# Kernel tuning notes

Measured on AMD Instinct MI355X. Metric: run time of the kernel, lower is better.

Reference implementation:

```python
import jax, jax.numpy as jnp
import numpy as np

B, T, I, H = 2048, 512, 9, 56


def _lstm_layer(x, w_ih, w_hh, b_ih, b_hh):
    """Single LSTM layer, batch_first x: [B, T, in] -> [B, T, H].
    PyTorch gate order: i, f, g, o."""
    # Precompute input projections for all timesteps in one GEMM: [B, T, 4H]
    xp = jnp.einsum('bti,gi->btg', x, w_ih) + b_ih + b_hh
    xp_t = jnp.transpose(xp, (1, 0, 2))  # [T, B, 4H]
    h0 = jnp.zeros((x.shape[0], w_hh.shape[1]), dtype=x.dtype)
    c0 = jnp.zeros_like(h0)

    def step(carry, xt):
        h, c = carry
        gates = xt + h @ w_hh.T  # [B, 4H]
        i, f, g, o = jnp.split(gates, 4, axis=-1)
        i = jax.nn.sigmoid(i)
        f = jax.nn.sigmoid(f)
        g = jnp.tanh(g)
        o = jax.nn.sigmoid(o)
        c = f * c + i * g
        h = o * jnp.tanh(c)
        return (h, c), h

    _, hs = jax.lax.scan(step, (h0, c0), xp_t)  # hs: [T, B, H]
    return jnp.transpose(hs, (1, 0, 2))  # [B, T, H]


def setup_inputs() -> dict:
    key = jax.random.key(0)
    ks = jax.random.split(key, 13)
    s_in = 1.0 / np.sqrt(H)
    inp = {
        'x': jax.random.normal(ks[0], (B, T, I), dtype=jnp.float32),
        'w_ih0': jax.random.uniform(ks[1], (4 * H, I), jnp.float32, -s_in, s_in),
        'w_hh0': jax.random.uniform(ks[2], (4 * H, H), jnp.float32, -s_in, s_in),
        'b_ih0': jax.random.uniform(ks[3], (4 * H,), jnp.float32, -s_in, s_in),
        'b_hh0': jax.random.uniform(ks[4], (4 * H,), jnp.float32, -s_in, s_in),
        'w_ih1': jax.random.uniform(ks[5], (4 * H, H), jnp.float32, -s_in, s_in),
        'w_hh1': jax.random.uniform(ks[6], (4 * H, H), jnp.float32, -s_in, s_in),
        'b_ih1': jax.random.uniform(ks[7], (4 * H,), jnp.float32, -s_in, s_in),
        'b_hh1': jax.random.uniform(ks[8], (4 * H,), jnp.float32, -s_in, s_in),
        'fc1_w': jax.random.uniform(ks[9], (H // 2, H), jnp.float32, -s_in, s_in),
        'fc1_b': jax.random.uniform(ks[10], (H // 2,), jnp.float32, -s_in, s_in),
        'fc2_w': jax.random.uniform(ks[11], (1, H // 2), jnp.float32, -0.2, 0.2),
        'fc2_b': jax.random.uniform(ks[12], (1,), jnp.float32, -0.2, 0.2),
    }
    return inp


def reference(x, w_ih0, w_hh0, b_ih0, b_hh0, w_ih1, w_hh1, b_ih1, b_hh1,
              fc1_w, fc1_b, fc2_w, fc2_b):
    h = _lstm_layer(x, w_ih0, w_hh0, b_ih0, b_hh0)   # [B, T, H]
    h = _lstm_layer(h, w_ih1, w_hh1, b_ih1, b_hh1)   # [B, T, H]
    last = h[:, -1]                                   # [B, H]
    y = jax.nn.relu(last @ fc1_w.T + fc1_b)           # [B, H//2]
    return y @ fc2_w.T + fc2_b                        # [B, 1]
```

## Files before the change

kernel.cpp:

```cpp
#include <hip/hip_runtime.h>
#include <stdint.h>

#define T_LEN 512
#define IN0   9
#define H     56
#define BG    8
#define NW    8
#define NTH   (NW * 64)
#define NBLK  256

typedef __attribute__((ext_vector_type(8))) short bfrag;
typedef __attribute__((ext_vector_type(4))) float ffrag;

#define MFMA(a,b,c) __builtin_amdgcn_mfma_f32_16x16x32_bf16((a),(b),(c),0,0,0)

__device__ __forceinline__ uint32_t bf16hi(float x) {
  uint32_t u = __float_as_uint(x);
  return (u + 0x7FFFu + ((u >> 16) & 1u)) & 0xFFFF0000u;
}
__device__ __forceinline__ void split_bf16(float x, short& hs, short& ls) {
  uint32_t hb = bf16hi(x);
  float lf = x - __uint_as_float(hb);
  hs = (short)(hb >> 16);
  ls = (short)(bf16hi(lf) >> 16);
}
__device__ __forceinline__ void split_bf16t(float x, short& hs, short& ls) {
  uint32_t hb = bf16hi(x);
  float lf = x - __uint_as_float(hb);
  hs = (short)(hb >> 16);
  ls = (short)(__float_as_uint(lf) >> 16);
}
__device__ __forceinline__ float dpp8(float v) {
  return __int_as_float(__builtin_amdgcn_update_dpp(0, __float_as_int(v), 0x128, 0xF, 0xF, true));
}
__device__ __forceinline__ float rcp_f(float v)  { return __builtin_amdgcn_rcpf(v); }
__device__ __forceinline__ float sigm_f(float v) { return rcp_f(1.0f + __expf(-v)); }
__device__ __forceinline__ float tanh_f(float v) { return 1.0f - 2.0f * rcp_f(1.0f + __expf(2.0f * v)); }

__global__ __launch_bounds__(NTH, 2)
void lstm_mfma12(const float* __restrict__ x,
                 const float* __restrict__ w_ih0, const float* __restrict__ w_hh0,
                 const float* __restrict__ b_ih0, const float* __restrict__ b_hh0,
                 const float* __restrict__ w_ih1, const float* __restrict__ w_hh1,
                 const float* __restrict__ b_ih1, const float* __restrict__ b_hh1,
                 const float* __restrict__ fc1_w, const float* __restrict__ fc1_b,
                 const float* __restrict__ fc2_w, const float* __restrict__ fc2_b,
                 float* __restrict__ out)
{
  __shared__ __align__(16) short hbufS[4 * 1024];
  __shared__ __align__(16) short xfS[T_LEN * 128];
  __shared__ __align__(16) float x8S[T_LEN * BG];
  __shared__ float sF[BG * H];
  __shared__ float sY[BG * 28];

  const int tid  = threadIdx.x;
  const int lane = tid & 63;
  const int w    = tid >> 6;
  const int c16  = lane & 15;
  const int quad = lane >> 4;

  const bool HASB = (w < 6);
  const int  sBi  = HASB ? (8 + w) : 0;

  for (int i = tid; i < 2048; i += NTH) ((int*)hbufS)[i] = 0;

  const int lay = (lane >> 3) & 1;
  const int b   = lane & 7;

  bfrag B0hA[2], B0lA[2], BuhA[2], BhhA[2];
  bfrag B0hB[2], B0lB[2], BuhB[2], BhhB[2];

#define LOADA(SUF, SIDX)                                                        \
  {                                                                             \
    const int np_ = 16 * (SIDX) + c16;                                          \
    const int jb_ = np_ >> 2, gb_ = np_ & 3;                                    \
    const int wrow_ = gb_ * H + jb_;                                            \
    _Pragma("unroll")                                                           \
    for (int s = 0; s < 2; ++s) {                                               \
      union { short sh[8]; bfrag v; } a0h, a0l, auh, ahh;                       \
      _Pragma("unroll")                                                         \
      for (int jj = 0; jj < 8; ++jj) {                                          \
        const int k = 32 * s + quad * 8 + jj;                                   \
        const float w0 = (k < H) ? w_hh0[wrow_ * H + k]                         \
                                 : w_ih0[wrow_ * IN0 + (k - 56)];               \
        const float wu = (k < H) ? w_ih1[wrow_ * H + k] : 0.0f;                 \
        const float wh = (k < H) ? w_hh1[wrow_ * H + k] : 0.0f;                 \
        split_bf16(w0, a0h.sh[jj], a0l.sh[jj]);                                 \
        short dum;                                                              \
        split_bf16(wu, auh.sh[jj], dum);                       \
        split_bf16(wh, ahh.sh[jj], dum);                                        \
      }                                                                         \
      B0h##SUF[s] = a0h.v; B0l##SUF[s] = a0l.v;                                 \
      Buh##SUF[s] = auh.v; Bhh##SUF[s] = ahh.v;                                 \
    }                                                                           \
  }

  LOADA(A, w)
  LOADA(B, sBi)
#undef LOADA

  const int j4A = 4 * w + quad;
  const int j4B = 4 * sBi + quad;
  const ffrag zerof = { 0.f, 0.f, 0.f, 0.f };

#define SETUPS(SUF, J4)                                                         \
  ffrag bias0f##SUF, bias1f##SUF;                                               \
  _Pragma("unroll")                                                             \
  for (int r = 0; r < 4; ++r) {                                                 \
    const float v0 = b_ih0[r * H + (J4)] + b_hh0[r * H + (J4)];                 \
    const float v1 = b_ih1[r * H + (J4)] + b_hh1[r * H + (J4)];                 \
    bias0f##SUF[r] = (c16 < 8) ? v0 : 0.0f;                                     \
    bias1f##SUF[r] = (c16 < 8) ? v1 : 0.0f;                                     \
  }                                                                             \
  float wx8a##SUF[4];                                                           \
  _Pragma("unroll")                                                             \
  for (int r = 0; r < 4; ++r)                                                   \
    wx8a##SUF[r] = lay ? w_ih0[(r * H + (J4)) * IN0 + 8] : 0.0f;                \
  const int kk##SUF = (J4) & 31;                                                \
  const int offE##SUF = ((J4) >> 5) * 512 + ((kk##SUF >> 3) * 16 + b) * 8       \
                        + (kk##SUF & 7);                                        \
  short* const hp0##SUF = hbufS + (lay ? 0 : 3 * 1024) + offE##SUF;             \
  short* const hp1##SUF = hbufS + (lay ? 1 * 1024 : 2 * 1024) + offE##SUF;

  SETUPS(A, j4A)
  SETUPS(B, j4B)
#undef SETUPS

  for (int item = tid; item < T_LEN * BG; item += NTH) {
    const int t  = item & (T_LEN - 1);
    const int bb = item >> 9;
    const float* xr = x + ((size_t)(blockIdx.x * BG + bb) * T_LEN + t) * IN0;
    union { short s[8]; bfrag v; } hi, lo;
    #pragma unroll
    for (int q = 0; q < 8; ++q) split_bf16t(xr[q], hi.s[q], lo.s[q]);
    *(bfrag*)((char*)xfS + (size_t)t * 256 + bb * 16)       = hi.v;
    *(bfrag*)((char*)xfS + (size_t)t * 256 + (bb + 8) * 16) = lo.v;
    x8S[t * 8 + bb] = xr[8];
  }

  const char* const hB = (const char*)hbufS;
  const char* const pU0_0 = hB + 2048 + lane * 16;
  const char* const pU0_1 = hB +        lane * 16;
  const char* const pH0_0 = hB + 4096 + lane * 16;
  const char* const pH1_0 = hB + 5120 + lane * 16;
  const char* const pH0_1 = hB + 6144 + lane * 16;
  const char* const pH1_1 = hB + 7168 + lane * 16;
  const char* pU1_0 = (quad == 3) ? ((const char*)xfS + 256 * 1 + c16 * 16)
                                  : (hB + 3072 + lane * 16);
  const char* pU1_1 = (quad == 3) ? ((const char*)xfS + 256 * 2 + c16 * 16)
                                  : (hB + 1024 + lane * 16);
  const char* px8_0 = (const char*)x8S + 32 * 1 + b * 4;
  const char* px8_1 = (const char*)x8S + 32 * 2 + b * 4;
  const int incU1 = (quad == 3) ? 512 : 0;

  float cstA = 0.f, cstB = 0.f;
  __syncthreads();

#define ACT0(A0, WX8, CST, HBP, X8V)                                            \
  {                                                                             \
    float s0[4];                                                                \
    _Pragma("unroll")                                                           \
    for (int r = 0; r < 4; ++r) s0[r] = A0[r] + dpp8(A0[r]);                    \
    if (lay) {                                                                  \
      const float gi = fmaf(WX8[0], X8V, s0[0]);                                \
      const float gf = fmaf(WX8[1], X8V, s0[1]);                                \
      const float gg = fmaf(WX8[2], X8V, s0[2]);                                \
      const float go = fmaf(WX8[3], X8V, s0[3]);                                \
      const float iv = sigm_f(gi), fv = sigm_f(gf);                             \
      const float gv = tanh_f(gg), ov = sigm_f(go);                             \
      CST = fmaf(fv, CST, iv * gv);                                             \
      const float hv = ov * tanh_f(CST);                                        \
      short hs, hl; split_bf16t(hv, hs, hl);                                    \
      (HBP)[0] = hs; (HBP)[64] = hl;                                            \
    }                                                                           \
  }

#define ACT1(A0A, A0B, AH, WX8, CST, HBP, X8V)                                  \
  {                                                                             \
    float sv[4];                                                                \
    _Pragma("unroll")                                                           \
    for (int r = 0; r < 4; ++r) {                                               \
      const float t0 = A0A[r] + A0B[r];                                         \
      const float uu = lay ? t0 : AH[r];                                        \
      const float vv = lay ? AH[r] : t0;                                        \
      sv[r] = uu + dpp8(vv);                                                    \
    }                                                                           \
    const float gi = fmaf(WX8[0], X8V, sv[0]);                                  \
    const float gf = fmaf(WX8[1], X8V, sv[1]);                                  \
    const float gg = fmaf(WX8[2], X8V, sv[2]);                                  \
    const float go = fmaf(WX8[3], X8V, sv[3]);                                  \
    const float iv = sigm_f(gi), fv = sigm_f(gf);                               \
    const float gv = tanh_f(gg), ov = sigm_f(go);                               \
    CST = fmaf(fv, CST, iv * gv);                                               \
    const float hv = ov * tanh_f(CST);                                          \
    short hs, hl; split_bf16t(hv, hs, hl);                                      \
    (HBP)[0] = hs; (HBP)[64] = hl;                                              \
  }

#define ACTL(AH, CST, J4)                                                       \
  {                                                                             \
    float s1[4];                                                                \
    _Pragma("unroll")                                                           \
    for (int r = 0; r < 4; ++r) s1[r] = AH[r] + dpp8(AH[r]);                    \
    if (lay == 0) {                                                             \
      const float iv = sigm_f(s1[0]), fv = sigm_f(s1[1]);                       \
      const float gv = tanh_f(s1[2]), ov = sigm_f(s1[3]);                       \
      CST = fmaf(fv, CST, iv * gv);                                             \
      sF[b * H + (J4)] = ov * tanh_f(CST);                                      \
    }                                                                           \
  }

  {
    const bfrag U0 = *(const bfrag*)(hB + lane * 16);
    const char* pU1p = (quad == 3) ? ((const char*)xfS + c16 * 16)
                                   : (hB + 1024 + lane * 16);
    const bfrag U1 = *(const bfrag*)pU1p;
    const float x8v = x8S[b];
    ffrag a0A = MFMA(B0hA[0], U0, bias0fA);
    a0A = MFMA(B0hA[1], U1, a0A);
    a0A = MFMA(B0lA[0], U0, a0A);
    a0A = MFMA(B0lA[1], U1, a0A);
    ACT0(a0A, wx8aA, cstA, hp1A, x8v)
    if (HASB) {
      ffrag a0B = MFMA(B0hB[0], U0, bias0fB);
      a0B = MFMA(B0hB[1], U1, a0B);
      a0B = MFMA(B0lB[0], U0, a0B);
      a0B = MFMA(B0lB[1], U1, a0B);
      ACT0(a0B, wx8aB, cstB, hp1B, x8v)
    }
    __syncthreads();
  }

#define REGION(RR, L0PART, LASTR)                                               \
  {                                                                             \
    const bfrag U0 = *(const bfrag*)pU0_##RR;                                   \
    const bfrag U1 = *(const bfrag*)pU1_##RR;                                   \
    const bfrag H0 = *(const bfrag*)pH0_##RR;                                   \
    const bfrag H1 = *(const bfrag*)pH1_##RR;                                   \
    ffrag a0aA, a0bA, a0aB, a0bB;                                               \
    float x8v = 0.0f;                                                           \
    if (L0PART) x8v = *(const float*)px8_##RR;                                  \
    __builtin_amdgcn_s_setprio(1);                                              \
    if (L0PART) {                                                               \
      a0aA = MFMA(B0hA[0], U0, bias0fA);                                        \
      a0bA = MFMA(B0lA[0], U0, zerof);                                          \
      a0aA = MFMA(B0hA[1], U1, a0aA);                                           \
      a0bA = MFMA(B0lA[1], U1, a0bA);                                           \
      if (HASB) {                                                               \
        a0aB = MFMA(B0hB[0], U0, bias0fB);                                      \
        a0bB = MFMA(B0lB[0], U0, zerof);                                        \
        a0aB = MFMA(B0hB[1], U1, a0aB);                                         \
        a0bB = MFMA(B0lB[1], U1, a0bB);                                         \
      }                                                                         \
    }                                                                           \
          \
    ffrag aHA = MFMA(BhhA[0], H0, bias1fA);                                     \
    aHA = MFMA(BhhA[1], H1, aHA);                                               \
    aHA = MFMA(BuhA[0], U0, aHA);                                               \
    aHA = MFMA(BuhA[1], U1, aHA);                                               \
    ffrag aHB;                                                                  \
    if (HASB) {                                                                 \
      aHB = MFMA(BhhB[0], H0, bias1fB);                                         \
      aHB = MFMA(BhhB[1], H1, aHB);                                             \
      aHB = MFMA(BuhB[0], U0, aHB);                                             \
      aHB = MFMA(BuhB[1], U1, aHB);                                             \
    }                                                                           \
    __builtin_amdgcn_s_setprio(0);                                              \
    if (!LASTR) {                                                               \
      ACT1(a0aA, a0bA, aHA, wx8aA, cstA, ((RR) == 0) ? hp0A : hp1A, x8v)        \
      if (HASB) {                                                               \
        ACT1(a0aB, a0bB, aHB, wx8aB, cstB, ((RR) == 0) ? hp0B : hp1B, x8v)      \
      }                                                                         \
    } else {                                                                    \
      ACTL(aHA, cstA, j4A)                                                      \
      if (HASB) { ACTL(aHB, cstB, j4B) }                                        \
    }                                                                           \
    __syncthreads();                                                            \
  }

  for (int it = 0; it < 255; ++it) {
    REGION(0, 1, 0)
    REGION(1, 1, 0)
    pU1_0 += incU1; pU1_1 += incU1;
    px8_0 += 64;    px8_1 += 64;
  }
  REGION(0, 1, 0)
  pU1_1 -= incU1;
  REGION(1, 0, 1)
#undef REGION
#undef ACT0
#undef ACT1
#undef ACTL

  if (tid < 28 * BG) {
    const int m  = tid >> 3;
    const int bb = tid & 7;
    float acc = fc1_b[m];
    const float4* w4 = (const float4*)(fc1_w + m * H);
    const float4* h4 = (const float4*)(sF + bb * H);
    #pragma unroll
    for (int qq = 0; qq < H / 4; ++qq) {
      const float4 wv4 = w4[qq], hv4 = h4[qq];
      acc = fmaf(wv4.x, hv4.x, acc);
      acc = fmaf(wv4.y, hv4.y, acc);
      acc = fmaf(wv4.z, hv4.z, acc);
      acc = fmaf(wv4.w, hv4.w, acc);
    }
    sY[bb * 28 + m] = fmaxf(acc, 0.0f);
  }
  __syncthreads();
  if (tid < BG) {
    float acc = fc2_b[0];
    #pragma unroll
    for (int m = 0; m < 28; ++m)
      acc = fmaf(fc2_w[m], sY[tid * 28 + m], acc);
    out[blockIdx.x * BG + tid] = acc;
  }
}

extern "C" void kernel_launch(void* const* d_in, const int* in_sizes, int n_in,
                              void* d_out, int out_size, void* d_ws, size_t ws_size,
                              hipStream_t stream)
{
  const float* x     = (const float*)d_in[0];
  const float* w_ih0 = (const float*)d_in[1];
  const float* w_hh0 = (const float*)d_in[2];
  const float* b_ih0 = (const float*)d_in[3];
  const float* b_hh0 = (const float*)d_in[4];
  const float* w_ih1 = (const float*)d_in[5];
  const float* w_hh1 = (const float*)d_in[6];
  const float* b_ih1 = (const float*)d_in[7];
  const float* b_hh1 = (const float*)d_in[8];
  const float* fc1_w = (const float*)d_in[9];
  const float* fc1_b = (const float*)d_in[10];
  const float* fc2_w = (const float*)d_in[11];
  const float* fc2_b = (const float*)d_in[12];
  float* out = (float*)d_out;

  lstm_mfma12<<<NBLK, NTH, 0, stream>>>(
      x, w_ih0, w_hh0, b_ih0, b_hh0, w_ih1, w_hh1, b_ih1, b_hh1,
      fc1_w, fc1_b, fc2_w, fc2_b, out);
}
```

Before: 476.1 us.

## Process 16 batch rows per block with two ping-ponged wave groups

New measurement: 1.448 ms. 3.04x slower.

```diff
diff --git a/kernel.cpp b/kernel.cpp
--- a/kernel.cpp
+++ b/kernel.cpp
@@ -4,10 +4,10 @@
 #define T_LEN 512
 #define IN0   9
 #define H     56
-#define BG    8
-#define NW    8
+#define BG    16
+#define NW    14
 #define NTH   (NW * 64)
-#define NBLK  256
+#define NBLK  (2048 / BG)
 
 typedef __attribute__((ext_vector_type(8))) short bfrag;
 typedef __attribute__((ext_vector_type(4))) float ffrag;
@@ -38,7 +38,7 @@
 __device__ __forceinline__ float tanh_f(float v) { return 1.0f - 2.0f * rcp_f(1.0f + __expf(2.0f * v)); }
 
 __global__ __launch_bounds__(NTH, 2)
-void lstm_mfma12(const float* __restrict__ x,
+void lstm_mfma16(const float* __restrict__ x,
                  const float* __restrict__ w_ih0, const float* __restrict__ w_hh0,
                  const float* __restrict__ b_ih0, const float* __restrict__ b_hh0,
                  const float* __restrict__ w_ih1, const float* __restrict__ w_hh1,
@@ -47,9 +47,9 @@
                  const float* __restrict__ fc2_w, const float* __restrict__ fc2_b,
                  float* __restrict__ out)
 {
-  __shared__ __align__(16) short hbufS[4 * 1024];
-  __shared__ __align__(16) short xfS[T_LEN * 128];
-  __shared__ __align__(16) float x8S[T_LEN * BG];
+  __shared__ __align__(16) short hbufS[2 * 4096];
+  __shared__ __align__(16) short xstgS[2 * 2 * 128];
+  __shared__ __align__(16) float x8S[BG * T_LEN];
   __shared__ float sF[BG * H];
   __shared__ float sY[BG * 28];
 
@@ -59,22 +59,23 @@
   const int c16  = lane & 15;
   const int quad = lane >> 4;
 
-  const bool HASB = (w < 6);
-  const int  sBi  = HASB ? (8 + w) : 0;
-
-  for (int i = tid; i < 2048; i += NTH) ((int*)hbufS)[i] = 0;
-
-  const int lay = (lane >> 3) & 1;
-  const int b   = lane & 7;
+  const int  grp = (w >= 7);
+  const int  wg  = grp ? (w - 7) : w;
+  const bool wgz = (wg == 0);
+  const int  lay = (lane >> 3) & 1;
+  const int  b   = lane & 7;
+  const int  bg16 = grp * 8 + b;
+  const int  sA = 2 * wg, sB = 2 * wg + 1;
+  const int  j4A = 4 * sA + quad, j4B = 4 * sB + quad;
+
+  for (int i = tid; i < 4096; i += NTH) ((int*)hbufS)[i] = 0;
 
   bfrag B0hA[2], B0lA[2], BuhA[2], BhhA[2];
   bfrag B0hB[2], B0lB[2], BuhB[2], BhhB[2];
-
-#define LOADA(SUF, SIDX)                                                        \
+#define LOADW(SUF, SIDX)                                                        \
   {                                                                             \
     const int np_ = 16 * (SIDX) + c16;                                          \
-    const int jb_ = np_ >> 2, gb_ = np_ & 3;                                    \
-    const int wrow_ = gb_ * H + jb_;                                            \
+    const int wrow_ = (np_ & 3) * H + (np_ >> 2);                               \
     _Pragma("unroll")                                                           \
     for (int s = 0; s < 2; ++s) {                                               \
       union { short sh[8]; bfrag v; } a0h, a0l, auh, ahh;                       \
@@ -94,15 +95,11 @@
       Buh##SUF[s] = auh.v; Bhh##SUF[s] = ahh.v;                                 \
     }                                                                           \
   }
-
-  LOADA(A, w)
-  LOADA(B, sBi)
-#undef LOADA
-
-  const int j4A = 4 * w + quad;
-  const int j4B = 4 * sBi + quad;
+  LOADW(A, sA)
+  LOADW(B, sB)
+#undef LOADW
+
   const ffrag zerof = { 0.f, 0.f, 0.f, 0.f };
-
 #define SETUPS(SUF, J4)                                                         \
   ffrag bias0f##SUF, bias1f##SUF;                                               \
   _Pragma("unroll")                                                             \
@@ -118,60 +115,86 @@
     wx8a##SUF[r] = lay ? w_ih0[(r * H + (J4)) * IN0 + 8] : 0.0f;                \
   const int kk##SUF = (J4) & 31;                                                \
   const int offE##SUF = ((J4) >> 5) * 512 + ((kk##SUF >> 3) * 16 + b) * 8       \
-                        + (kk##SUF & 7);                                        \
-  short* const hp0##SUF = hbufS + (lay ? 0 : 3 * 1024) + offE##SUF;             \
-  short* const hp1##SUF = hbufS + (lay ? 1 * 1024 : 2 * 1024) + offE##SUF;
-
+                        + (kk##SUF & 7);
   SETUPS(A, j4A)
   SETUPS(B, j4B)
 #undef SETUPS
 
-  for (int item = tid; item < T_LEN * BG; item += NTH) {
-    const int t  = item & (T_LEN - 1);
-    const int bb = item >> 9;
-    const float* xr = x + ((size_t)(blockIdx.x * BG + bb) * T_LEN + t) * IN0;
-    union { short s[8]; bfrag v; } hi, lo;
-    #pragma unroll
-    for (int q = 0; q < 8; ++q) split_bf16t(xr[q], hi.s[q], lo.s[q]);
-    *(bfrag*)((char*)xfS + (size_t)t * 256 + bb * 16)       = hi.v;
-    *(bfrag*)((char*)xfS + (size_t)t * 256 + (bb + 8) * 16) = lo.v;
-    x8S[t * 8 + bb] = xr[8];
-  }
-
-  const char* const hB = (const char*)hbufS;
-  const char* const pU0_0 = hB + 2048 + lane * 16;
-  const char* const pU0_1 = hB +        lane * 16;
-  const char* const pH0_0 = hB + 4096 + lane * 16;
-  const char* const pH1_0 = hB + 5120 + lane * 16;
-  const char* const pH0_1 = hB + 6144 + lane * 16;
-  const char* const pH1_1 = hB + 7168 + lane * 16;
-  const char* pU1_0 = (quad == 3) ? ((const char*)xfS + 256 * 1 + c16 * 16)
-                                  : (hB + 3072 + lane * 16);
-  const char* pU1_1 = (quad == 3) ? ((const char*)xfS + 256 * 2 + c16 * 16)
-                                  : (hB + 1024 + lane * 16);
-  const char* px8_0 = (const char*)x8S + 32 * 1 + b * 4;
-  const char* px8_1 = (const char*)x8S + 32 * 2 + b * 4;
-  const int incU1 = (quad == 3) ? 512 : 0;
-
+  const int gBs = grp * 4096;
+  short* const hwA0 = hbufS + gBs + (lay ? 0 * 1024 : 2048 + 1024) + offEA;
+  short* const hwA1 = hbufS + gBs + (lay ? 1 * 1024 : 2048 + 0)    + offEA;
+  short* const hwB0 = hbufS + gBs + (lay ? 0 * 1024 : 2048 + 1024) + offEB;
+  short* const hwB1 = hbufS + gBs + (lay ? 1 * 1024 : 2048 + 0)    + offEB;
+
+  const char* const hBb = (const char*)hbufS + grp * 8192;
+  const char* const xsb = (const char*)xstgS + grp * 512;
+  const char* const pU0_0 = hBb + 1 * 2048 + lane * 16;
+  const char* const pU0_1 = hBb + 0 * 2048 + lane * 16;
+  const char* const pU1_0 = (quad == 3) ? (xsb + 0 * 256 + c16 * 16) : (pU0_0 + 1024);
+  const char* const pU1_1 = (quad == 3) ? (xsb + 1 * 256 + c16 * 16) : (pU0_1 + 1024);
+  const char* const pH0_0 = hBb + 4096 + 0 * 2048 + lane * 16;
+  const char* const pH0_1 = hBb + 4096 + 1 * 2048 + lane * 16;
+
+  const int sb_ = (lane >> 2) & 7, se_ = lane & 3;
+  uint32_t* const xw_0 = (uint32_t*)((char*)xstgS + grp * 512 + 0 * 256 + sb_ * 16 + 4 * se_);
+  uint32_t* const xw_1 = (uint32_t*)((char*)xstgS + grp * 512 + 1 * 256 + sb_ * 16 + 4 * se_);
+  const float* xgp = x + ((size_t)(blockIdx.x * BG + grp * 8 + sb_) * T_LEN + 1) * IN0 + 2 * se_;
+
+  for (int item = tid; item < BG * T_LEN; item += NTH) {
+    const int bb = item >> 9, t = item & (T_LEN - 1);
+    x8S[item] = x[((size_t)(blockIdx.x * BG + bb) * T_LEN + t) * IN0 + 8];
+  }
+  if (wgz && lane < 32) {
+    const float* g0 = x + ((size_t)(blockIdx.x * BG + grp * 8 + sb_) * T_LEN) * IN0 + 2 * se_;
+    const float xa = g0[0], xb = g0[1];
+    short ah_, al_, bh_, bl_;
+    split_bf16t(xa, ah_, al_); split_bf16t(xb, bh_, bl_);
+    xw_0[0]  = (uint16_t)ah_ | ((uint32_t)(uint16_t)bh_ << 16);
+    xw_0[32] = (uint16_t)al_ | ((uint32_t)(uint16_t)bl_ << 16);
+  }
+
+  const float* const px8 = x8S + (size_t)bg16 * T_LEN;
   float cstA = 0.f, cstB = 0.f;
-  __syncthreads();
-
-#define ACT0(A0, WX8, CST, HBP, X8V)                                            \
-  {                                                                             \
-    float s0[4];                                                                \
-    _Pragma("unroll")                                                           \
-    for (int r = 0; r < 4; ++r) s0[r] = A0[r] + dpp8(A0[r]);                    \
-    if (lay) {                                                                  \
-      const float gi = fmaf(WX8[0], X8V, s0[0]);                                \
-      const float gf = fmaf(WX8[1], X8V, s0[1]);                                \
-      const float gg = fmaf(WX8[2], X8V, s0[2]);                                \
-      const float go = fmaf(WX8[3], X8V, s0[3]);                                \
-      const float iv = sigm_f(gi), fv = sigm_f(gf);                             \
-      const float gv = tanh_f(gg), ov = sigm_f(go);                             \
-      CST = fmaf(fv, CST, iv * gv);                                             \
-      const float hv = ov * tanh_f(CST);                                        \
-      short hs, hl; split_bf16t(hv, hs, hl);                                    \
-      (HBP)[0] = hs; (HBP)[64] = hl;                                            \
+  ffrag aaA, abA, ahA, aaB, abB, ahB;
+  __syncthreads();
+
+#define P1(P, L0P, L1P, STGF)                                                   \
+  {                                                                             \
+    float stga = 0.f, stgb = 0.f;                                               \
+    if (STGF) { if (wgz && lane < 32) { stga = xgp[0]; stgb = xgp[1]; } }       \
+    const bfrag U0 = *(const bfrag*)pU0_##P;                                    \
+    const bfrag U1 = *(const bfrag*)pU1_##P;                                    \
+    if (L0P) {                                                                  \
+      aaA = MFMA(B0hA[0], U0, bias0fA);                                         \
+      abA = MFMA(B0lA[0], U0, zerof);                                           \
+      aaA = MFMA(B0hA[1], U1, aaA);                                             \
+      abA = MFMA(B0lA[1], U1, abA);                                             \
+      aaB = MFMA(B0hB[0], U0, bias0fB);                                         \
+      abB = MFMA(B0lB[0], U0, zerof);                                           \
+      aaB = MFMA(B0hB[1], U1, aaB);                                             \
+      abB = MFMA(B0lB[1], U1, abB);                                             \
+    }                                                                           \
+    if (L1P) {                                                                  \
+      const bfrag H0 = *(const bfrag*)pH0_##P;                                  \
+      const bfrag H1 = *(const bfrag*)(pH0_##P + 1024);                         \
+      ahA = MFMA(BhhA[0], H0, bias1fA);                                         \
+      ahA = MFMA(BhhA[1], H1, ahA);                                             \
+      ahA = MFMA(BuhA[0], U0, ahA);                                             \
+      ahA = MFMA(BuhA[1], U1, ahA);                                             \
+      ahB = MFMA(BhhB[0], H0, bias1fB);                                         \
+      ahB = MFMA(BhhB[1], H1, ahB);                                             \
+      ahB = MFMA(BuhB[0], U0, ahB);                                             \
+      ahB = MFMA(BuhB[1], U1, ahB);                                             \
+    }                                                                           \
+    if (STGF) {                                                                 \
+      if (wgz && lane < 32) {                                                   \
+        short ah_, al_, bh_, bl_;                                               \
+        split_bf16t(stga, ah_, al_); split_bf16t(stgb, bh_, bl_);               \
+        uint32_t* xw = (P) ? xw_0 : xw_1;          \
+        xw[0]  = (uint16_t)ah_ | ((uint32_t)(uint16_t)bh_ << 16);               \
+        xw[32] = (uint16_t)al_ | ((uint32_t)(uint16_t)bl_ << 16);               \
+        xgp += IN0;                                                             \
+      }                                                                         \
     }                                                                           \
   }
 
@@ -185,10 +208,10 @@
       const float vv = lay ? AH[r] : t0;                                        \
       sv[r] = uu + dpp8(vv);                                                    \
     }                                                                           \
-    const float gi = fmaf(WX8[0], X8V, sv[0]);                                  \
-    const float gf = fmaf(WX8[1], X8V, sv[1]);                                  \
-    const float gg = fmaf(WX8[2], X8V, sv[2]);                                  \
-    const float go = fmaf(WX8[3], X8V, sv[3]);                                  \
+    const float gi = fmaf(WX8[0], (X8V), sv[0]);                                \
+    const float gf = fmaf(WX8[1], (X8V), sv[1]);                                \
+    const float gg = fmaf(WX8[2], (X8V), sv[2]);                                \
+    const float go = fmaf(WX8[3], (X8V), sv[3]);                                \
     const float iv = sigm_f(gi), fv = sigm_f(gf);                               \
     const float gv = tanh_f(gg), ov = sigm_f(go);                               \
     CST = fmaf(fv, CST, iv * gv);                                               \
@@ -197,104 +220,115 @@
     (HBP)[0] = hs; (HBP)[64] = hl;                                              \
   }
 
-#define ACTL(AH, CST, J4)                                                       \
+#define P2(Q, TT)                                                               \
+  {                                                                             \
+    const float x8v = px8[(TT)];                                                \
+    ACT1(aaA, abA, ahA, wx8aA, cstA, (Q) ? hwA1 : hwA0, x8v)                    \
+    ACT1(aaB, abB, ahB, wx8aB, cstB, (Q) ? hwB1 : hwB0, x8v)                    \
+  }
+
+#define P2_FIRST                                                                \
+  {                                                                             \
+    const float x8v = px8[0];                                                   \
+    if (lay) {                                                                  \
+      _Pragma("unroll")                                                         \
+      for (int tt2 = 0; tt2 < 1; ++tt2) {                                       \
+        float s0[4];                                                            \
+        _Pragma("unroll")                                                       \
+        for (int r = 0; r < 4; ++r) {                                           \
+          const float t0 = aaA[r] + abA[r];                                     \
+          s0[r] = t0 + dpp8(t0);                                                \
+        }                                                                       \
+        const float gi = fmaf(wx8aA[0], x8v, s0[0]);                            \
+        const float gf = fmaf(wx8aA[1], x8v, s0[1]);                            \
+        const float gg = fmaf(wx8aA[2], x8v, s0[2]);                            \
+        const float go = fmaf(wx8aA[3], x8v, s0[3]);                            \
+        const float iv = sigm_f(gi), fv = sigm_f(gf);                           \
+        const float gv = tanh_f(gg), ov = sigm_f(go);                           \
+        cstA = fmaf(fv, cstA, iv * gv);                                         \
+        const float hv = ov * tanh_f(cstA);                                     \
+        short hs, hl; split_bf16t(hv, hs, hl);                                  \
+        hwA0[0] = hs; hwA0[64] = hl;                                            \
+        float s1[4];                                                            \
+        _Pragma("unroll")                                                       \
+        for (int r = 0; r < 4; ++r) {                                           \
+          const float t1 = aaB[r] + abB[r];                                     \
+          s1[r] = t1 + dpp8(t1);                                                \
+        }                                                                       \
+        const float gi2 = fmaf(wx8aB[0], x8v, s1[0]);                           \
+        const float gf2 = fmaf(wx8aB[1], x8v, s1[1]);                           \
+        const float gg2 = fmaf(wx8aB[2], x8v, s1[2]);                           \
+        const float go2 = fmaf(wx8aB[3], x8v, s1[3]);                           \
+        const float iv2 = sigm_f(gi2), fv2 = sigm_f(gf2);                       \
+        const float gv2 = tanh_f(gg2), ov2 = sigm_f(go2);                       \
+        cstB = fmaf(fv2, cstB, iv2 * gv2);                                      \
+        const float hv2 = ov2 * tanh_f(cstB);                                   \
+        short hs2, hl2; split_bf16t(hv2, hs2, hl2);                             \
+        hwB0[0] = hs2; hwB0[64] = hl2;                                          \
+      }                                                                         \
+    } else {                                                                    \
+      float dmy = dpp8(aaA[0] + abA[0]) + dpp8(aaB[0] + abB[0]);                \
+      asm volatile("" :: "v"(dmy));      \
+    }                                                                           \
+  }
+
+#define PFIN                                                                    \
   {                                                                             \
     float s1[4];                                                                \
     _Pragma("unroll")                                                           \
-    for (int r = 0; r < 4; ++r) s1[r] = AH[r] + dpp8(AH[r]);                    \
+    for (int r = 0; r < 4; ++r) s1[r] = ahA[r] + dpp8(ahA[r]);                  \
+    float s2[4];                                                                \
+    _Pragma("unroll")                                                           \
+    for (int r = 0; r < 4; ++r) s2[r] = ahB[r] + dpp8(ahB[r]);                  \
     if (lay == 0) {                                                             \
-      const float iv = sigm_f(s1[0]), fv = sigm_f(s1[1]);                       \
-      const float gv = tanh_f(s1[2]), ov = sigm_f(s1[3]);                       \
-      CST = fmaf(fv, CST, iv * gv);                                             \
-      sF[b * H + (J4)] = ov * tanh_f(CST);                                      \
-    }                                                                           \
-  }
-
-  {
-    const bfrag U0 = *(const bfrag*)(hB + lane * 16);
-    const char* pU1p = (quad == 3) ? ((const char*)xfS + c16 * 16)
-                                   : (hB + 1024 + lane * 16);
-    const bfrag U1 = *(const bfrag*)pU1p;
-    const float x8v = x8S[b];
-    ffrag a0A = MFMA(B0hA[0], U0, bias0fA);
-    a0A = MFMA(B0hA[1], U1, a0A);
-    a0A = MFMA(B0lA[0], U0, a0A);
-    a0A = MFMA(B0lA[1], U1, a0A);
-    ACT0(a0A, wx8aA, cstA, hp1A, x8v)
-    if (HASB) {
-      ffrag a0B = MFMA(B0hB[0], U0, bias0fB);
-      a0B = MFMA(B0hB[1], U1, a0B);
-      a0B = MFMA(B0lB[0], U0, a0B);
-      a0B = MFMA(B0lB[1], U1, a0B);
-      ACT0(a0B, wx8aB, cstB, hp1B, x8v)
-    }
+      { const float iv = sigm_f(s1[0]), fv = sigm_f(s1[1]);                     \
+        const float gv = tanh_f(s1[2]), ov = sigm_f(s1[3]);                     \
+        cstA = fmaf(fv, cstA, iv * gv);                                         \
+        sF[bg16 * H + j4A] = ov * tanh_f(cstA); }                               \
+      { const float iv = sigm_f(s2[0]), fv = sigm_f(s2[1]);                     \
+        const float gv = tanh_f(s2[2]), ov = sigm_f(s2[3]);                     \
+        cstB = fmaf(fv, cstB, iv * gv);                                         \
+        sF[bg16 * H + j4B] = ov * tanh_f(cstB); }                               \
+    }                                                                           \
+  }
+
+  if (!grp) { P1(0, 1, 0, 1) }
+  __syncthreads();
+  if (!grp) { P2_FIRST } else { P1(0, 1, 0, 1) }
+  __syncthreads();
+
+  int t1 = 1;
+  for (int it = 0; it < 255; ++it) {
+    if (!grp) { P1(1, 1, 1, 1) } else { P2(0, t1 - 1) }
     __syncthreads();
-  }
-
-#define REGION(RR, L0PART, LASTR)                                               \
-  {                                                                             \
-    const bfrag U0 = *(const bfrag*)pU0_##RR;                                   \
-    const bfrag U1 = *(const bfrag*)pU1_##RR;                                   \
-    const bfrag H0 = *(const bfrag*)pH0_##RR;                                   \
-    const bfrag H1 = *(const bfrag*)pH1_##RR;                                   \
-    ffrag a0aA, a0bA, a0aB, a0bB;                                               \
-    float x8v = 0.0f;                                                           \
-    if (L0PART) x8v = *(const float*)px8_##RR;                                  \
-    __builtin_amdgcn_s_setprio(1);                                              \
-    if (L0PART) {                                                               \
-      a0aA = MFMA(B0hA[0], U0, bias0fA);                                        \
-      a0bA = MFMA(B0lA[0], U0, zerof);                                          \
-      a0aA = MFMA(B0hA[1], U1, a0aA);                                           \
-      a0bA = MFMA(B0lA[1], U1, a0bA);                                           \
-      if (HASB) {                                                               \
-        a0aB = MFMA(B0hB[0], U0, bias0fB);                                      \
-        a0bB = MFMA(B0lB[0], U0, zerof);                                        \
-        a0aB = MFMA(B0hB[1], U1, a0aB);                                         \
-        a0bB = MFMA(B0lB[1], U1, a0bB);                                         \
-      }                                                                         \
-    }                                                                           \
-          \
-    ffrag aHA = MFMA(BhhA[0], H0, bias1fA);                                     \
-    aHA = MFMA(BhhA[1], H1, aHA);                                               \
-    aHA = MFMA(BuhA[0], U0, aHA);                                               \
-    aHA = MFMA(BuhA[1], U1, aHA);                                               \
-    ffrag aHB;                                                                  \
-    if (HASB) {                                                                 \
-      aHB = MFMA(BhhB[0], H0, bias1fB);                                         \
-      aHB = MFMA(BhhB[1], H1, aHB);                                             \
-      aHB = MFMA(BuhB[0], U0, aHB);                                             \
-      aHB = MFMA(BuhB[1], U1, aHB);                                             \
-    }                                                                           \
-    __builtin_amdgcn_s_setprio(0);                                              \
-    if (!LASTR) {                                                               \
-      ACT1(a0aA, a0bA, aHA, wx8aA, cstA, ((RR) == 0) ? hp0A : hp1A, x8v)        \
-      if (HASB) {                                                               \
-        ACT1(a0aB, a0bB, aHB, wx8aB, cstB, ((RR) == 0) ? hp0B : hp1B, x8v)      \
-      }                                                                         \
-    } else {                                                                    \
-      ACTL(aHA, cstA, j4A)                                                      \
-      if (HASB) { ACTL(aHB, cstB, j4B) }                                        \
-    }                                                                           \
-    __syncthreads();                                                            \
-  }
-
-  for (int it = 0; it < 255; ++it) {
-    REGION(0, 1, 0)
-    REGION(1, 1, 0)
-    pU1_0 += incU1; pU1_1 += incU1;
-    px8_0 += 64;    px8_1 += 64;
-  }
-  REGION(0, 1, 0)
-  pU1_1 -= incU1;
-  REGION(1, 0, 1)
-#undef REGION
-#undef ACT0
+    if (!grp) { P2(1, t1) } else { P1(1, 1, 1, 1) }
+    __syncthreads();
+    if (!grp) { P1(0, 1, 1, 1) } else { P2(1, t1) }
+    __syncthreads();
+    if (!grp) { P2(0, t1 + 1) } else { P1(0, 1, 1, 1) }
+    __syncthreads();
+    t1 += 2;
+  }
+  if (!grp) { P1(1, 1, 1, 0) } else { P2(0, t1 - 1) }
+  __syncthreads();
+  if (!grp) { P2(1, t1) } else { P1(1, 1, 1, 0) }
+  __syncthreads();
+  if (!grp) { P1(0, 0, 1, 0) } else { P2(1, t1) }
+  __syncthreads();
+  if (!grp) { PFIN } else { P1(0, 0, 1, 0) }
+  __syncthreads();
+  if (grp) { PFIN }
+  __syncthreads();
+
+#undef P1
+#undef P2
+#undef P2_FIRST
+#undef PFIN
 #undef ACT1
-#undef ACTL
 
   if (tid < 28 * BG) {
-    const int m  = tid >> 3;
-    const int bb = tid & 7;
+    const int m  = tid >> 4;
+    const int bb = tid & 15;
     float acc = fc1_b[m];
     const float4* w4 = (const float4*)(fc1_w + m * H);
     const float4* h4 = (const float4*)(sF + bb * H);
@@ -337,7 +371,7 @@
   const float* fc2_b = (const float*)d_in[12];
   float* out = (float*)d_out;
 
-  lstm_mfma12<<<NBLK, NTH, 0, stream>>>(
+  lstm_mfma16<<<NBLK, NTH, 0, stream>>>(
       x, w_ih0, w_hh0, b_ih0, b_hh0, w_ih1, w_hh1, b_ih1, b_hh1,
       fc1_w, fc1_b, fc2_w, fc2_b, out);
 }
```
